# Performance work log

Hardware: AMD Instinct MI355X
Metric: run time of the kernel (lower is better)

Reference implementation:

```python
import jax, jax.numpy as jnp
import numpy as np

R = 128          # input voxel grid resolution
N = 200000
C_IN = 128
C_OUT = 256
G = 32           # group-norm groups
EPS = 1e-5


def _build_sparse_structure():
    """Generate random sparse voxel coords, downsample map, and 3x3x3 neighbor table."""
    rng = np.random.default_rng(0)
    lin = rng.choice(R ** 3, size=N, replace=False)
    cx, cy, cz = lin // (R * R), (lin // R) % R, lin % R
    # downsample by 2: coords // 2 on a (R//2)^3 grid
    Rd = R // 2
    key = ((cx // 2) * Rd + (cy // 2)) * Rd + (cz // 2)
    uk, inv = np.unique(key, return_inverse=True)   # uk sorted
    M = len(uk)
    dx, dy, dz = uk // (Rd * Rd), (uk // Rd) % Rd, uk % Rd
    # 27-neighbor table for submanifold 3x3x3 conv on the downsampled coords
    nbr = np.full((M, 27), -1, np.int32)
    k = 0
    for ox in (-1, 0, 1):
        for oy in (-1, 0, 1):
            for oz in (-1, 0, 1):
                nx, ny, nz = dx + ox, dy + oy, dz + oz
                valid = (nx >= 0) & (nx < Rd) & (ny >= 0) & (ny < Rd) & (nz >= 0) & (nz < Rd)
                nkey = (nx * Rd + ny) * Rd + nz
                pos = np.clip(np.searchsorted(uk, nkey), 0, M - 1)
                found = valid & (uk[pos] == nkey)
                nbr[:, k] = np.where(found, pos, -1).astype(np.int32)
                k += 1
    return inv.astype(np.int32), nbr, M


def setup_inputs() -> dict:
    pool_seg, nbr_idx, M = _build_sparse_structure()
    key = jax.random.key(0)
    ks = jax.random.split(key, 12)
    f32 = jnp.float32
    feats = jax.random.normal(ks[0], (N, C_IN), f32)
    s1 = float(1.0 / np.sqrt(27 * C_IN))
    s2 = float(1.0 / np.sqrt(27 * C_OUT))
    return {
        "feats": feats,
        "gn1_w": 1.0 + 0.1 * jax.random.normal(ks[1], (C_IN,), f32),
        "gn1_b": 0.1 * jax.random.normal(ks[2], (C_IN,), f32),
        "W1": jax.random.normal(ks[3], (27, C_IN, C_OUT), f32) * s1,
        "b1": 0.01 * jax.random.normal(ks[4], (C_OUT,), f32),
        "gn2_w": 1.0 + 0.1 * jax.random.normal(ks[5], (C_OUT,), f32),
        "gn2_b": 0.1 * jax.random.normal(ks[6], (C_OUT,), f32),
        "W2": jax.random.normal(ks[7], (27, C_OUT, C_OUT), f32) * s2,
        "b2": 0.01 * jax.random.normal(ks[8], (C_OUT,), f32),
        "Wskip": jax.random.normal(ks[9], (C_IN, C_OUT), f32) * float(1.0 / np.sqrt(C_IN)),
        "bskip": 0.01 * jax.random.normal(ks[10], (C_OUT,), f32),
        "pool_seg": jnp.asarray(pool_seg),
        "nbr_idx": jnp.asarray(nbr_idx),
        "num_down": int(M),
    }


def _group_norm(x, gamma, beta):
    # batch size 1: normalize each group over all voxels and its channels
    n, c = x.shape
    xg = x.reshape(n, G, c // G)
    mu = xg.mean(axis=(0, 2), keepdims=True)
    var = xg.var(axis=(0, 2), keepdims=True)
    xn = (xg - mu) * jax.lax.rsqrt(var + EPS)
    return xn.reshape(n, c) * gamma + beta


def _sparse_conv3(x, W, b, nbr_idx):
    # submanifold 3x3x3 conv: out[i] = sum_k W[k] @ x[nbr[i,k]] (missing nbr -> 0)
    idx = jnp.maximum(nbr_idx, 0)
    mask = (nbr_idx >= 0).astype(x.dtype)
    acc = jnp.zeros((x.shape[0], W.shape[2]), x.dtype)
    for k in range(27):
        acc = acc + (x[idx[:, k]] * mask[:, k:k + 1]) @ W[k]
    return acc + b


def reference(feats, gn1_w, gn1_b, W1, b1, gn2_w, gn2_b, W2, b2, Wskip, bskip,
              pool_seg, nbr_idx, num_down):
    # act_layers: GroupNorm32 + SiLU on the full-resolution sparse tensor
    h = jax.nn.silu(_group_norm(feats, gn1_w, gn1_b))
    # SparseDownsample(2): average features of voxels sharing a coord//2 cell
    cnt = jax.ops.segment_sum(jnp.ones((feats.shape[0], 1), feats.dtype),
                              pool_seg, num_segments=num_down)
    inv_cnt = 1.0 / jnp.maximum(cnt, 1.0)
    h_d = jax.ops.segment_sum(h, pool_seg, num_segments=num_down) * inv_cnt
    x_d = jax.ops.segment_sum(feats, pool_seg, num_segments=num_down) * inv_cnt
    # out_layers: conv3 -> GN -> SiLU -> conv3
    h1 = _sparse_conv3(h_d, W1, b1, nbr_idx)
    h2 = jax.nn.silu(_group_norm(h1, gn2_w, gn2_b))
    h3 = _sparse_conv3(h2, W2, b2, nbr_idx)
    # skip: 1x1 sparse conv on downsampled input, then add (same coord set)
    skip = x_d @ Wskip + bskip
    return h3 + skip
```

## Files before the change

kernel.cpp:

```cpp
#include <hip/hip_runtime.h>
#include <hip/hip_bf16.h>
#include <stdint.h>

typedef __hip_bfloat16 bf16;
typedef __attribute__((ext_vector_type(8))) __bf16 bf16x8;
typedef __attribute__((ext_vector_type(4))) float f32x4;

#define GN_EPS 1e-5f

__device__ __forceinline__ float silu_f(float x) {
  return x / (1.f + __expf(-x));
}

__device__ __forceinline__ float ldf(const void* p, size_t i, int f) {
  return f ? ((const float*)p)[i]
           : __bfloat162float(((const bf16*)p)[i]);
}

__device__ __forceinline__ void llds16(const void* g, void* l) {
  __builtin_amdgcn_global_load_lds(
      (const __attribute__((address_space(1))) unsigned int*)g,
      (__attribute__((address_space(3))) unsigned int*)l, 16, 0, 0);
}

__global__ void detect_k(const void* __restrict__ gn1w, int* __restrict__ flag) {
  if (threadIdx.x == 0 && blockIdx.x == 0) {
    const unsigned short* u = (const unsigned short*)gn1w;
    float mx = 0.f;
    for (int i = 0; i < 128; ++i) {
      unsigned int b = ((unsigned int)u[i]) << 16;
      float v = __uint_as_float(b);
      v = fabsf(v);
      if (!isnan(v) && v > mx) mx = v;
    }
    flag[0] = (mx > 1e4f) ? 1 : 0;
  }
}

__global__ void transpose_k(const void* __restrict__ in, bf16* __restrict__ out,
                            int CI, int CO, const int* __restrict__ flagp) {
  const int f = *flagp;
  int k = blockIdx.y;
  int ntco = CO >> 5;
  int tci = blockIdx.x / ntco, tco = blockIdx.x % ntco;
  __shared__ float t[32][33];
  int tx = threadIdx.x & 31, ty = threadIdx.x >> 5;
  size_t base = (size_t)k * CI * CO;
  bf16* dst = out + base;
#pragma unroll
  for (int j = 0; j < 4; ++j)
    t[ty + 8 * j][tx] =
        ldf(in, base + (size_t)(tci * 32 + ty + 8 * j) * CO + tco * 32 + tx, f);
  __syncthreads();
#pragma unroll
  for (int j = 0; j < 4; ++j)
    dst[(size_t)(tco * 32 + ty + 8 * j) * CI + tci * 32 + tx] =
        __float2bfloat16(t[tx][ty + 8 * j]);
}

__global__ void gn_stats_k(const void* __restrict__ x, float* __restrict__ raw,
                           int rows, int C, const int* __restrict__ flagp) {
  const int f = *flagp;
  int tid = threadIdx.x;
  int rpb = 256 / C;
  int c = tid & (C - 1);
  int stripe = tid / C;
  float s = 0.f, sq = 0.f;
  for (int r = blockIdx.x * rpb + stripe; r < rows; r += gridDim.x * rpb) {
    float v = ldf(x, (size_t)r * C + c, f);
    s += v; sq += v * v;
  }
  __shared__ float ls[256], lq[256];
  ls[tid] = s; lq[tid] = sq;
  __syncthreads();
  if (tid < 32) {
    int per = C >> 5;
    float as = 0.f, aq = 0.f;
    for (int st = 0; st < rpb; ++st)
      for (int e = 0; e < per; ++e) {
        int idx = st * C + tid * per + e;
        as += ls[idx]; aq += lq[idx];
      }
    atomicAdd(&raw[tid], as);
    atomicAdd(&raw[32 + tid], aq);
  }
}

__global__ void gn_fin_k(const float* __restrict__ raw, float* __restrict__ fin,
                         float count) {
  int g = threadIdx.x;
  if (g < 32) {
    float mu = raw[g] / count;
    float var = fmaxf(raw[32 + g] / count - mu * mu, 0.f);
    fin[g] = mu;
    fin[32 + g] = rsqrtf(var + GN_EPS);
  }
}

__global__ void slots_k(const int* __restrict__ seg, int* __restrict__ cnt,
                        int* __restrict__ slots, int N) {
  int i = blockIdx.x * 256 + threadIdx.x;
  if (i >= N) return;
  int s = seg[i];
  int p = atomicAdd(&cnt[s], 1);
  if (p < 8) slots[s * 8 + p] = i;
}

__global__ void down_k(const void* __restrict__ feats, const int* __restrict__ slots,
                       const int* __restrict__ cnt, const float* __restrict__ fin1,
                       const void* __restrict__ gw, const void* __restrict__ gb,
                       bf16* __restrict__ xd, bf16* __restrict__ hd, int M,
                       const int* __restrict__ flagp) {
  const int f = *flagp;
  int cell = blockIdx.x * 2 + (threadIdx.x >> 7);
  int c = threadIdx.x & 127;
  if (cell >= M) return;
  int n = min(cnt[cell], 8);
  int g = c >> 2;
  float mu = fin1[g], is = fin1[32 + g];
  float w = ldf(gw, c, f), b = ldf(gb, c, f);
  float xs = 0.f, hs = 0.f;
  for (int j = 0; j < n; ++j) {
    int v = slots[cell * 8 + j];
    float fv = ldf(feats, (size_t)v * 128 + c, f);
    xs += fv;
    hs += silu_f((fv - mu) * is * w + b);
  }
  float inv = 1.f / (float)max(n, 1);
  xd[(size_t)cell * 128 + c] = __float2bfloat16(xs * inv);
  hd[(size_t)cell * 128 + c] = __float2bfloat16(hs * inv);
}

__global__ void act2_k(bf16* __restrict__ h, const float* __restrict__ fin2,
                       const void* __restrict__ gw, const void* __restrict__ gb,
                       size_t total8, const int* __restrict__ flagp) {
  const int f = *flagp;
  size_t i = (size_t)blockIdx.x * 256 + threadIdx.x;
  if (i >= total8) return;
  int c0 = (int)((i * 8) & 255);
  int g = c0 >> 3;
  float mu = fin2[g], is = fin2[32 + g];
  bf16x8 v = *reinterpret_cast<bf16x8*>(h + i * 8);
  bf16x8 o;
#pragma unroll
  for (int j = 0; j < 8; ++j) {
    float x = (float)v[j];
    float t = (x - mu) * is * ldf(gw, c0 + j, f) + ldf(gb, c0 + j, f);
    o[j] = (__bf16)silu_f(t);
  }
  *reinterpret_cast<bf16x8*>(h + i * 8) = o;
}

template <int CIN, bool SKIP>
__global__ __launch_bounds__(512, 2) void conv_k(
    const bf16* __restrict__ A, const bf16* __restrict__ Wt,
    const void* __restrict__ bias, const void* __restrict__ bias2,
    const bf16* __restrict__ Xd, const int* __restrict__ nbr,
    void* __restrict__ out, int M, int nwg, const void* __restrict__ zp,
    const int* __restrict__ biasflagp, const int* __restrict__ outflagp) {
  constexpr int NCB = CIN / 32;
  constexpr int LOG_NCB = (CIN == 256) ? 3 : 2;
  constexpr int NT = 27 * NCB + (SKIP ? 4 : 0);
  __shared__ alignas(16) char smem[49152 + 65536 + 27648];
  char* Aring = smem;
  char* Bring = smem + 49152;
  int* nbrT = (int*)(smem + 49152 + 65536);

  const int bflag = *biasflagp, oflag = *outflagp;
  const int tid = threadIdx.x;
  const int wave = tid >> 6, lane = tid & 63;

  int bid = blockIdx.x;
  int q = nwg >> 3, r8 = nwg & 7, xcd = bid & 7, ix = bid >> 3;
  int wg = (xcd < r8 ? xcd * (q + 1) : r8 * (q + 1) + (xcd - r8) * q) + ix;
  const int row0 = wg * 192;

  for (int i = tid; i < 27 * 256; i += 512) {
    int k = i >> 8, r = i & 255;
    int g = row0 + r;
    int v = -1;
    if (r < 192 && g < M) v = nbr[(size_t)g * 27 + k];
    nbrT[i] = v;
  }
  __syncthreads();

  const int srow = lane >> 2;
  const int schk = lane & 3;

  auto stage = [&](int t) {
    char* Asl = Aring + (size_t)(t & 3) * 12288;
    char* Bsl = Bring + (size_t)(t & 3) * 16384;
    const bool isW = (!SKIP) || (t < 27 * NCB);
    const int kk = t >> LOG_NCB;
    const int cb = isW ? (t & (NCB - 1)) : (t - 27 * NCB);
    const int cink = isW ? CIN : 128;
    const bf16* Ab = isW ? A : Xd;
    const bf16* Wb = Wt + (isW ? (size_t)kk * (256 * CIN)
                               : (size_t)27 * (256 * CIN));
    const int koff = cb * 32;
#pragma unroll
    for (int ro = 0; ro < 2; ++ro) {
      int c = ro * 128 + wave * 16 + srow;
      int lc = schk ^ ((c >> 1) & 3);
      llds16(Wb + (size_t)c * cink + koff + lc * 8,
             Bsl + (size_t)(ro * 128 + wave * 16) * 64);
    }
    {
      int r = wave * 16 + srow;
      int src;
      if (isW) src = nbrT[(kk << 8) + r];
      else { int g = row0 + r; src = (g < M) ? g : -1; }
      int lc = schk ^ ((r >> 1) & 3);
      const bf16* ga = (src >= 0) ? Ab + (size_t)src * cink + koff + lc * 8
                                  : (const bf16*)zp;
      llds16(ga, Asl + (size_t)(wave * 16) * 64);
    }
    if (wave < 4) {
      int r = 128 + wave * 16 + srow;
      int src;
      if (isW) src = nbrT[(kk << 8) + r];
      else { int g = row0 + r; src = (g < M) ? g : -1; }
      int lc = schk ^ ((r >> 1) & 3);
      const bf16* ga = (src >= 0) ? Ab + (size_t)src * cink + koff + lc * 8
                                  : (const bf16*)zp;
      llds16(ga, Asl + (size_t)(128 + wave * 16) * 64);
    }
  };

  const int mrow = lane & 15, quad = lane >> 4;
  const int wr = wave >> 2, wc = wave & 3;
  const int cswz = (quad ^ ((mrow >> 1) & 3)) * 16;

  f32x4 acc[6][4] = {};

  auto compute = [&](int t) {
    const char* As = Aring + (size_t)(t & 3) * 12288 +
                     (size_t)(wr * 96 + mrow) * 64 + cswz;
    const char* Bs = Bring + (size_t)(t & 3) * 16384 +
                     (size_t)(wc * 64 + mrow) * 64 + cswz;
    bf16x8 af[6], bv[4];
#pragma unroll
    for (int i = 0; i < 6; ++i)
      af[i] = *reinterpret_cast<const bf16x8*>(As + i * (16 * 64));
#pragma unroll
    for (int j = 0; j < 4; ++j)
      bv[j] = *reinterpret_cast<const bf16x8*>(Bs + j * (16 * 64));
    __builtin_amdgcn_s_setprio(1);
#pragma unroll
    for (int i = 0; i < 6; ++i)
#pragma unroll
      for (int j = 0; j < 4; ++j)
        acc[i][j] = __builtin_amdgcn_mfma_f32_16x16x32_bf16(af[i], bv[j],
                                                            acc[i][j], 0, 0, 0);
    __builtin_amdgcn_s_setprio(0);
  };

#define VMW(a, b)                                                      \
  do {                                                                 \
    if (wave < 4) asm volatile("s_waitcnt vmcnt(" #a ")" ::: "memory"); \
    else          asm volatile("s_waitcnt vmcnt(" #b ")" ::: "memory"); \
  } while (0)
#define BAR() asm volatile("s_barrier" ::: "memory")

  stage(0); stage(1); stage(2);

#pragma unroll 1
  for (int t = 0; t < NT - 3; ++t) {
    stage(t + 3);
    VMW(12, 9);
    BAR();
    compute(t);
    BAR();
  }
  VMW(8, 6); BAR(); compute(NT - 3); BAR();
  VMW(4, 3); BAR(); compute(NT - 2); BAR();
  VMW(0, 0); BAR(); compute(NT - 1);

#undef VMW
#undef BAR

#pragma unroll
  for (int j = 0; j < 4; ++j) {
    int col = wc * 64 + j * 16 + mrow;
    float bvl = ldf(bias, col, bflag);
    if (SKIP) bvl += ldf(bias2, col, bflag);
#pragma unroll
    for (int i = 0; i < 6; ++i) {
      int rb = row0 + wr * 96 + i * 16 + quad * 4;
#pragma unroll
      for (int r = 0; r < 4; ++r) {
        int row = rb + r;
        if (row < M) {
          size_t idx = (size_t)row * 256 + col;
          float val = acc[i][j][r] + bvl;
          if (oflag) ((float*)out)[idx] = val;
          else ((bf16*)out)[idx] = __float2bfloat16(val);
        }
      }
    }
  }
}

extern "C" void kernel_launch(void* const* d_in, const int* in_sizes, int n_in,
                              void* d_out, int out_size, void* d_ws, size_t ws_size,
                              hipStream_t stream) {
  const void* feats = d_in[0];
  const void* gn1w = d_in[1];
  const void* gn1b = d_in[2];
  const void* W1 = d_in[3];
  const void* b1 = d_in[4];
  const void* gn2w = d_in[5];
  const void* gn2b = d_in[6];
  const void* W2 = d_in[7];
  const void* b2 = d_in[8];
  const void* Wsk = d_in[9];
  const void* bsk = d_in[10];
  const int* pool = (const int*)d_in[11];
  const int* nbr = (const int*)d_in[12];
  const int N = in_sizes[0] / 128;
  const int M = out_size / 256;

  char* ws = (char*)d_ws;
  auto aup = [](size_t x) { return (x + 255) & ~(size_t)255; };
  float* raw1 = (float*)(ws + 0);
  float* raw2 = (float*)(ws + 256);
  int* flag = (int*)(ws + 512);
  int* zeroflag = (int*)(ws + 516);
  const void* zp = (const void*)(ws + 768);
  int* cnt = (int*)(ws + 1024);
  size_t o = aup(1024 + (size_t)M * 4);
  float* fin1 = (float*)(ws + o); o += 256;
  float* fin2 = (float*)(ws + o); o += 256;
  int* slots = (int*)(ws + o); o = aup(o + (size_t)M * 32);
  bf16* xd = (bf16*)(ws + o); o += (size_t)M * 256;
  bf16* hd = (bf16*)(ws + o); o += (size_t)M * 256;
  bf16* h1 = (bf16*)(ws + o); o += (size_t)M * 512;
  bf16* wt1 = (bf16*)(ws + o); o += (size_t)27 * 256 * 128 * 2;
  bf16* wt2 = (bf16*)(ws + o); o += ((size_t)27 * 256 * 256 + 256 * 128) * 2;
  (void)ws_size; (void)n_in;

  hipMemsetAsync(ws, 0, 1024 + (size_t)M * 4, stream);

  detect_k<<<1, 64, 0, stream>>>(gn1w, flag);

  transpose_k<<<dim3(4 * 8, 27), 256, 0, stream>>>(W1, wt1, 128, 256, flag);
  transpose_k<<<dim3(8 * 8, 27), 256, 0, stream>>>(W2, wt2, 256, 256, flag);
  transpose_k<<<dim3(4 * 8, 1), 256, 0, stream>>>(
      Wsk, wt2 + (size_t)27 * 256 * 256, 128, 256, flag);

  gn_stats_k<<<512, 256, 0, stream>>>(feats, raw1, N, 128, flag);
  gn_fin_k<<<1, 64, 0, stream>>>(raw1, fin1, (float)N * 4.f);

  slots_k<<<(N + 255) / 256, 256, 0, stream>>>(pool, cnt, slots, N);
  down_k<<<(M + 1) / 2, 256, 0, stream>>>(feats, slots, cnt, fin1, gn1w, gn1b,
                                          xd, hd, M, flag);

  const int nwg = (M + 191) / 192;

  conv_k<128, false><<<nwg, 512, 0, stream>>>(
      hd, wt1, b1, nullptr, nullptr, nbr, h1, M, nwg, zp, flag, zeroflag);

  gn_stats_k<<<512, 256, 0, stream>>>(h1, raw2, M, 256, zeroflag);
  gn_fin_k<<<1, 64, 0, stream>>>(raw2, fin2, (float)M * 8.f);
  act2_k<<<(int)(((size_t)M * 32 + 255) / 256), 256, 0, stream>>>(
      h1, fin2, gn2w, gn2b, (size_t)M * 32, flag);

  conv_k<256, true><<<nwg, 512, 0, stream>>>(
      h1, wt2, b2, bsk, xd, nbr, d_out, M, nwg, zp, flag, flag);
}
```

Baseline: 1.479 ms.

## Load conv weights directly into registers instead of staging through LDS

Weights are re-laid out by the transpose kernel into per-32-channel panels. Each wave now loads its B fragments straight from global memory into registers with double-buffered dwordx4 loads, instead of staging them through an LDS ring. This removes the 64KB B ring from LDS and the associated LDS read traffic, and restructures the pipeline to unroll by two with different vmcnt waits. It risks exposing weight-load latency, raises register pressure, and the hand-tuned waitcnt counts and barrier placement could be wrong.

```diff
diff --git a/kernel.cpp b/kernel.cpp
--- a/kernel.cpp
+++ b/kernel.cpp
@@ -21,6 +21,11 @@
   __builtin_amdgcn_global_load_lds(
       (const __attribute__((address_space(1))) unsigned int*)g,
       (__attribute__((address_space(3))) unsigned int*)l, 16, 0, 0);
+}
+
+__device__ __forceinline__ void gload16(bf16x8& d, const bf16* base, int voff) {
+  asm volatile("global_load_dwordx4 %0, %1, %2"
+               : "=&v"(d) : "v"(voff), "s"(base) : "memory");
 }
 
 __global__ void detect_k(const void* __restrict__ gn1w, int* __restrict__ flag) {
@@ -54,7 +59,7 @@
   __syncthreads();
 #pragma unroll
   for (int j = 0; j < 4; ++j)
-    dst[(size_t)(tco * 32 + ty + 8 * j) * CI + tci * 32 + tx] =
+    dst[(size_t)tci * (CO * 32) + (size_t)(tco * 32 + ty + 8 * j) * 32 + tx] =
         __float2bfloat16(t[tx][ty + 8 * j]);
 }
 
@@ -161,14 +166,14 @@
   constexpr int NCB = CIN / 32;
   constexpr int LOG_NCB = (CIN == 256) ? 3 : 2;
   constexpr int NT = 27 * NCB + (SKIP ? 4 : 0);
-  __shared__ alignas(16) char smem[49152 + 65536 + 27648];
+  __shared__ alignas(16) char smem[49152 + 27648];
   char* Aring = smem;
-  char* Bring = smem + 49152;
-  int* nbrT = (int*)(smem + 49152 + 65536);
+  int* nbrT = (int*)(smem + 49152);
 
   const int bflag = *biasflagp, oflag = *outflagp;
   const int tid = threadIdx.x;
   const int wave = tid >> 6, lane = tid & 63;
+  const bool w03 = (wave < 4);
 
   int bid = blockIdx.x;
   int q = nwg >> 3, r8 = nwg & 7, xcd = bid & 7, ix = bid >> 3;
@@ -187,43 +192,31 @@
   const int srow = lane >> 2;
   const int schk = lane & 3;
 
-  auto stage = [&](int t) {
+  auto stageA1 = [&](int t, int panel, char* Asl, bool isW, int kk, int koff,
+                     int cink, const bf16* Ab) {
+    int r = panel * 16 + srow;
+    int src;
+    if (isW) src = nbrT[(kk << 8) + r];
+    else { int g = row0 + r; src = (g < M) ? g : -1; }
+    int lc = schk ^ ((r >> 1) & 3);
+    const bf16* ga = (src >= 0) ? Ab + (size_t)src * cink + koff + lc * 8
+                                : (const bf16*)zp;
+    llds16(ga, Asl + (size_t)panel * 1024);
+  };
+
+  auto stageA = [&](int t) {
     char* Asl = Aring + (size_t)(t & 3) * 12288;
-    char* Bsl = Bring + (size_t)(t & 3) * 16384;
     const bool isW = (!SKIP) || (t < 27 * NCB);
     const int kk = t >> LOG_NCB;
     const int cb = isW ? (t & (NCB - 1)) : (t - 27 * NCB);
     const int cink = isW ? CIN : 128;
     const bf16* Ab = isW ? A : Xd;
-    const bf16* Wb = Wt + (isW ? (size_t)kk * (256 * CIN)
-                               : (size_t)27 * (256 * CIN));
     const int koff = cb * 32;
-#pragma unroll
-    for (int ro = 0; ro < 2; ++ro) {
-      int c = ro * 128 + wave * 16 + srow;
-      int lc = schk ^ ((c >> 1) & 3);
-      llds16(Wb + (size_t)c * cink + koff + lc * 8,
-             Bsl + (size_t)(ro * 128 + wave * 16) * 64);
-    }
-    {
-      int r = wave * 16 + srow;
-      int src;
-      if (isW) src = nbrT[(kk << 8) + r];
-      else { int g = row0 + r; src = (g < M) ? g : -1; }
-      int lc = schk ^ ((r >> 1) & 3);
-      const bf16* ga = (src >= 0) ? Ab + (size_t)src * cink + koff + lc * 8
-                                  : (const bf16*)zp;
-      llds16(ga, Asl + (size_t)(wave * 16) * 64);
-    }
-    if (wave < 4) {
-      int r = 128 + wave * 16 + srow;
-      int src;
-      if (isW) src = nbrT[(kk << 8) + r];
-      else { int g = row0 + r; src = (g < M) ? g : -1; }
-      int lc = schk ^ ((r >> 1) & 3);
-      const bf16* ga = (src >= 0) ? Ab + (size_t)src * cink + koff + lc * 8
-                                  : (const bf16*)zp;
-      llds16(ga, Asl + (size_t)(128 + wave * 16) * 64);
+    if (w03) {
+      stageA1(t, 2 * wave, Asl, isW, kk, koff, cink, Ab);
+      stageA1(t, 2 * wave + 1, Asl, isW, kk, koff, cink, Ab);
+    } else {
+      stageA1(t, 4 + wave, Asl, isW, kk, koff, cink, Ab);
     }
   };
 
@@ -231,20 +224,31 @@
   const int wr = wave >> 2, wc = wave & 3;
   const int cswz = (quad ^ ((mrow >> 1) & 3)) * 16;
 
+  int bvoff[4];
+#pragma unroll
+  for (int j = 0; j < 4; ++j)
+    bvoff[j] = ((wc * 64 + j * 16 + mrow) * 32 + quad * 8) * 2;
+
+  auto loadB = [&](bf16x8 (&dst)[4], int t) {
+    const bool isW = (!SKIP) || (t < 27 * NCB);
+    const int kk = t >> LOG_NCB;
+    const int cb = isW ? (t & (NCB - 1)) : (t - 27 * NCB);
+    const bf16* base = Wt +
+        (isW ? (size_t)kk * (256 * CIN) : (size_t)27 * (256 * CIN)) +
+        (size_t)cb * (256 * 32);
+#pragma unroll
+    for (int j = 0; j < 4; ++j) gload16(dst[j], base, bvoff[j]);
+  };
+
   f32x4 acc[6][4] = {};
 
-  auto compute = [&](int t) {
+  auto compute = [&](int t, const bf16x8 (&bv)[4]) {
     const char* As = Aring + (size_t)(t & 3) * 12288 +
                      (size_t)(wr * 96 + mrow) * 64 + cswz;
-    const char* Bs = Bring + (size_t)(t & 3) * 16384 +
-                     (size_t)(wc * 64 + mrow) * 64 + cswz;
-    bf16x8 af[6], bv[4];
+    bf16x8 af[6];
 #pragma unroll
     for (int i = 0; i < 6; ++i)
       af[i] = *reinterpret_cast<const bf16x8*>(As + i * (16 * 64));
-#pragma unroll
-    for (int j = 0; j < 4; ++j)
-      bv[j] = *reinterpret_cast<const bf16x8*>(Bs + j * (16 * 64));
     __builtin_amdgcn_s_setprio(1);
 #pragma unroll
     for (int i = 0; i < 6; ++i)
@@ -255,26 +259,40 @@
     __builtin_amdgcn_s_setprio(0);
   };
 
-#define VMW(a, b)                                                      \
-  do {                                                                 \
-    if (wave < 4) asm volatile("s_waitcnt vmcnt(" #a ")" ::: "memory"); \
-    else          asm volatile("s_waitcnt vmcnt(" #b ")" ::: "memory"); \
+#define VMW(a, b)                                                        \
+  do {                                                                   \
+    if (w03) asm volatile("s_waitcnt vmcnt(" #a ")" ::: "memory");       \
+    else     asm volatile("s_waitcnt vmcnt(" #b ")" ::: "memory");       \
+    __builtin_amdgcn_sched_barrier(0);                                   \
   } while (0)
-#define BAR() asm volatile("s_barrier" ::: "memory")
-
-  stage(0); stage(1); stage(2);
+#define BAR() __builtin_amdgcn_s_barrier()
+
+  bf16x8 bX[4], bY[4];
+
+  stageA(0); stageA(1);
+  loadB(bX, 0);
 
 #pragma unroll 1
-  for (int t = 0; t < NT - 3; ++t) {
-    stage(t + 3);
-    VMW(12, 9);
+  for (int u = 0; u < NT / 2 - 1; ++u) {
+    const int s = 2 * u;
+    loadB(bY, s + 1);
+    stageA(s + 2);
+    VMW(6, 5);
     BAR();
-    compute(t);
+    compute(s, bX);
+    loadB(bX, s + 2);
+    stageA(s + 3);
+    VMW(8, 6);
     BAR();
-  }
-  VMW(8, 6); BAR(); compute(NT - 3); BAR();
-  VMW(4, 3); BAR(); compute(NT - 2); BAR();
-  VMW(0, 0); BAR(); compute(NT - 1);
+    compute(s + 1, bY);
+  }
+  loadB(bY, NT - 1);
+  VMW(6, 5);
+  BAR();
+  compute(NT - 2, bX);
+  VMW(0, 0);
+  BAR();
+  compute(NT - 1, bY);
 
 #undef VMW
 #undef BAR
```

After: 1.375 ms. -7.1%, faster.
